# Kernel tuning notes

Hardware: AMD Instinct MI355X
Metric: run time of the kernel (lower is better)

## Reference

```python
import jax, jax.numpy as jnp
import numpy as np

N_HEAD = 16
N_EMBD = 1024
HEAD_DIM = N_EMBD // N_HEAD


def setup_inputs() -> dict:
    key = jax.random.key(0)
    k1, k2, k3 = jax.random.split(key, 3)
    B, T, C = 2, 2048, N_EMBD
    x = jax.random.normal(k1, (B, T, C), dtype=jnp.float32)
    # Linear weights stored as (in, out); torch nn.Linear weight is (out,in), y = x @ W.T.
    # We store the already-transposed form so reference does x @ w.
    w_attn = jax.random.normal(k2, (C, 3 * C), dtype=jnp.float32) * (1.0 / np.sqrt(C))
    w_proj = jax.random.normal(k3, (C, C), dtype=jnp.float32) * (1.0 / np.sqrt(C))
    return {"x": x, "w_attn": w_attn, "w_proj": w_proj}


def reference(x, w_attn, w_proj):
    B, T, C = x.shape
    qkv = x @ w_attn                          # [B,T,3C]
    q, k, v = jnp.split(qkv, 3, axis=2)
    # [B,T,C] -> [B,H,T,D]
    def heads(t):
        return t.reshape(B, T, N_HEAD, HEAD_DIM).transpose(0, 2, 1, 3)
    q, k, v = heads(q), heads(k), heads(v)
    scale = 1.0 / np.sqrt(HEAD_DIM)
    att = jnp.einsum('bhqd,bhkd->bhqk', q, k) * scale  # [B,H,T,T]
    causal = jnp.tril(jnp.ones((T, T), dtype=bool))
    att = jnp.where(causal, att, -jnp.inf)
    att = jax.nn.softmax(att, axis=-1)
    y = jnp.einsum('bhqk,bhkd->bhqd', att, v)          # [B,H,T,D]
    y = y.transpose(0, 2, 1, 3).reshape(B, T, C)
    return y @ w_proj
```

## Files before the change

### kernel.cpp

```cpp
#include <hip/hip_runtime.h>
#include <hip/hip_bf16.h>
#include <stdint.h>

typedef unsigned short u16;
typedef unsigned int u32;
typedef unsigned long long u64;
typedef float f32x4 __attribute__((ext_vector_type(4)));
typedef float f32x16 __attribute__((ext_vector_type(16)));
typedef short bf16x8 __attribute__((ext_vector_type(8)));
typedef u32 u32x4 __attribute__((ext_vector_type(4)));

#define MFMA(a, b, c) __builtin_amdgcn_mfma_f32_16x16x32_bf16((a), (b), (c), 0, 0, 0)
#define MFMA32(a, b, c) __builtin_amdgcn_mfma_f32_32x32x16_bf16((a), (b), (c), 0, 0, 0)

__device__ __forceinline__ void gll16(const void* g, void* lds) {
  __builtin_amdgcn_global_load_lds(
      (const __attribute__((address_space(1))) u32*)(uintptr_t)g,
      (__attribute__((address_space(3))) u32*)(uintptr_t)lds, 16, 0, 0);
}

__device__ __forceinline__ u16 f2b(float f) {
  union { __hip_bfloat16 h; u16 u; } cv;
  cv.h = __float2bfloat16(f);
  return cv.u;
}
__device__ __forceinline__ float b2f(u16 b) {
  union { u32 u; float f; } cv;
  cv.u = (u32)b << 16;
  return cv.f;
}
__device__ __forceinline__ u32 cvtpk(float lo, float hi) {
  u32 r;
  asm("v_cvt_pk_bf16_f32 %0, %1, %2" : "=v"(r) : "v"(lo), "v"(hi));
  return r;
}

__device__ __forceinline__ int sw(int r) { return ((r ^ (r >> 3)) & 7) << 4; }

__global__ __launch_bounds__(256) void k_cvt(const float* __restrict__ in,
                                             u16* __restrict__ out, int n4) {
  int i = blockIdx.x * 256 + threadIdx.x;
  if (i >= n4) return;
  const float4 v = reinterpret_cast<const float4*>(in)[i];
  u32 lo = (u32)f2b(v.x) | ((u32)f2b(v.y) << 16);
  u32 hi = (u32)f2b(v.z) | ((u32)f2b(v.w) << 16);
  reinterpret_cast<uint2*>(out)[i] = make_uint2(lo, hi);
}

__global__ __launch_bounds__(256) void k_trcvt(const float* __restrict__ in,
                                               u16* __restrict__ out, int R, int C) {
  __shared__ float tile[64][65];
  const int tid = threadIdx.x;
  const int r0 = blockIdx.y * 64, c0 = blockIdx.x * 64;
  const int tr = tid >> 4;
  const int tc4 = (tid & 15) * 4;
#pragma unroll
  for (int i = 0; i < 4; ++i) {
    const float4 v = *reinterpret_cast<const float4*>(
        &in[(size_t)(r0 + i * 16 + tr) * C + c0 + tc4]);
    tile[i * 16 + tr][tc4 + 0] = v.x;
    tile[i * 16 + tr][tc4 + 1] = v.y;
    tile[i * 16 + tr][tc4 + 2] = v.z;
    tile[i * 16 + tr][tc4 + 3] = v.w;
  }
  __syncthreads();
#pragma unroll
  for (int i = 0; i < 4; ++i) {
    const int c = i * 16 + tr;
    const int r4 = tc4;
    u32 lo = (u32)f2b(tile[r4 + 0][c]) | ((u32)f2b(tile[r4 + 1][c]) << 16);
    u32 hi = (u32)f2b(tile[r4 + 2][c]) | ((u32)f2b(tile[r4 + 3][c]) << 16);
    *reinterpret_cast<uint2*>(&out[(size_t)(c0 + c) * R + r0 + r4]) =
        make_uint2(lo, hi);
  }
}

template <int F32OUT>
__global__ __launch_bounds__(256) void k_gemm(const u16* __restrict__ A,
                                              const u16* __restrict__ Bt,
                                              void* __restrict__ Cout,
                                              int M, int N, int K) {
  __shared__ u16 As[128 * 32];
  __shared__ u16 Bs[128 * 32];
  const int tid = threadIdx.x;
  const int lane = tid & 63;
  const int w = tid >> 6;
  const int wm = w >> 1, wn = w & 1;
  const int l15 = lane & 15, lg = lane >> 4;
  const int brow = blockIdx.y * 128;
  const int bcol = blockIdx.x * 128;

  f32x4 acc[4][4] = {};

  const int r0 = tid >> 2;
  const int k8 = (tid & 3) * 8;
  const u16* Ag0 = A + (size_t)(brow + r0) * K + k8;
  const u16* Ag1 = A + (size_t)(brow + 64 + r0) * K + k8;
  const u16* Bg0 = Bt + (size_t)(bcol + r0) * K + k8;
  const u16* Bg1 = Bt + (size_t)(bcol + 64 + r0) * K + k8;
  u16* Asl0 = As + tid * 8;
  u16* Asl1 = As + 2048 + tid * 8;
  u16* Bsl0 = Bs + tid * 8;
  u16* Bsl1 = Bs + 2048 + tid * 8;

  for (int k0 = 0; k0 < K; k0 += 32) {
    gll16(Ag0 + k0, Asl0);
    gll16(Ag1 + k0, Asl1);
    gll16(Bg0 + k0, Bsl0);
    gll16(Bg1 + k0, Bsl1);
    __syncthreads();
    bf16x8 a[4], b[4];
#pragma unroll
    for (int m = 0; m < 4; ++m)
      a[m] = *(const bf16x8*)&As[(wm * 64 + m * 16 + l15) * 32 + lg * 8];
#pragma unroll
    for (int n = 0; n < 4; ++n)
      b[n] = *(const bf16x8*)&Bs[(wn * 64 + n * 16 + l15) * 32 + lg * 8];
#pragma unroll
    for (int m = 0; m < 4; ++m)
#pragma unroll
      for (int n = 0; n < 4; ++n)
        acc[m][n] = MFMA(a[m], b[n], acc[m][n]);
    __syncthreads();
  }

#pragma unroll
  for (int m = 0; m < 4; ++m) {
    const int row = brow + wm * 64 + m * 16 + lg * 4;
#pragma unroll
    for (int n = 0; n < 4; ++n) {
      const int col = bcol + wn * 64 + n * 16 + l15;
#pragma unroll
      for (int r = 0; r < 4; ++r) {
        const float v = acc[m][n][r];
        if (F32OUT)
          ((float*)Cout)[(size_t)(row + r) * N + col] = v;
        else
          ((u16*)Cout)[(size_t)(row + r) * N + col] = f2b(v);
      }
    }
  }
}

__global__ __launch_bounds__(512, 1) void k_attn(const u16* __restrict__ qkv,
                                                 u16* __restrict__ y) {
  __shared__ u16 Kl[3][64 * 64];
  __shared__ u16 Vt[2][64 * 64];
  __shared__ float Om[4][64][33];
  __shared__ float Lm[4][2][32];
  const int tid = threadIdx.x;
  const int lane = tid & 63;
  const int w = tid >> 6;
  const int qsub = w & 3, tsub = w >> 2;
  const int l31 = lane & 31, hi = lane >> 5;

  const int lin = blockIdx.x;
  const int xcd = lin & 7;
  const int idx = lin >> 3;
  const int bh = xcd * 4 + (idx >> 3);
  const int pidx = idx & 7;
  const int b = bh >> 4, h = bh & 15;

  const u16* Qg = qkv + (size_t)(b * 2048) * 3072 + h * 64;
  const u16* Kg = Qg + 1024;
  const u16* Vg = Qg + 2048;

  const int srow = tid >> 3;
  const int scol = (((tid & 7) * 16) ^ sw(srow)) >> 1;
  const bool vstage = (tid < 256);
  const int t2 = (tid & 255) >> 3;
  const int d8 = (tid & 7) * 8;

  bf16x8 vone;
#pragma unroll
  for (int j = 0; j < 8; ++j) vone[j] = (short)0x3F80;

  const int trow = tsub * 32 + l31;
  int koff[4];
#pragma unroll
  for (int ks = 0; ks < 4; ++ks)
    koff[ks] = trow * 128 + (((ks * 16 + hi * 8) * 2) ^ sw(trow));
  int voff[2][2];
#pragma unroll
  for (int db = 0; db < 2; ++db) {
    const int dl = db * 32 + l31;
#pragma unroll
    for (int ks = 0; ks < 2; ++ks)
      voff[db][ks] = dl * 128 + (((tsub * 32 + ks * 16 + hi * 8) * 2) ^ sw(dl));
  }

  for (int pass = 0; pass < 2; ++pass) {
    const int qi = pass ? (15 - pidx) : pidx;
    const int nt = 2 * (qi + 1);
    const int qb = qi * 128;
    const int qrow = qb + qsub * 32 + l31;

    bf16x8 aq[4];
#pragma unroll
    for (int ks = 0; ks < 4; ++ks) {
      bf16x8 v = *(const bf16x8*)&Qg[(size_t)qrow * 3072 + ks * 16 + hi * 8];
#pragma unroll
      for (int j = 0; j < 8; ++j)
        v[j] = (short)f2b(b2f((u16)v[j]) * 0.18033688011112042f);
      aq[ks] = v;
    }

    f32x16 acc0 = {}, acc1 = {}, accl = {};

    bf16x8 va0, va1;
    {
      bf16x8 v00, v01;
      if (vstage) {
        v00 = *(const bf16x8*)&Vg[(size_t)(2 * t2) * 3072 + d8];
        v01 = *(const bf16x8*)&Vg[(size_t)(2 * t2 + 1) * 3072 + d8];
        va0 = *(const bf16x8*)&Vg[(size_t)(64 + 2 * t2) * 3072 + d8];
        va1 = *(const bf16x8*)&Vg[(size_t)(64 + 2 * t2 + 1) * 3072 + d8];
      }
      gll16(Kg + (size_t)srow * 3072 + scol, (u16*)Kl[0] + tid * 8);
      gll16(Kg + (size_t)(64 + srow) * 3072 + scol, (u16*)Kl[1] + tid * 8);
      if (vstage) {
#pragma unroll
        for (int j = 0; j < 8; ++j) {
          const int d = d8 + j;
          const u32 val = (u32)(u16)v00[j] | ((u32)(u16)v01[j] << 16);
          *(u32*)((char*)Vt[0] + ((d * 128 + t2 * 4) ^ sw(d))) = val;
        }
      }
    }
    asm volatile("s_waitcnt vmcnt(1) lgkmcnt(0)" ::: "memory");
    __builtin_amdgcn_s_barrier();
    __builtin_amdgcn_sched_barrier(0);

    const char* kR = (const char*)Kl[0];
    const char* kN = (const char*)Kl[1];
    char* kN2 = (char*)Kl[2];
    const char* vR = (const char*)Vt[0];
    char* vW = (char*)Vt[1];

    for (int t = 0; t < nt; ++t) {
      const int tf = (t + 2 < 31 ? t + 2 : 31);
      bf16x8 vf0, vf1;
      if (vstage) {
        vf0 = *(const bf16x8*)&Vg[(size_t)(tf * 64 + 2 * t2) * 3072 + d8];
        vf1 = *(const bf16x8*)&Vg[(size_t)(tf * 64 + 2 * t2 + 1) * 3072 + d8];
      }
      gll16(Kg + (size_t)(tf * 64 + srow) * 3072 + scol, (u16*)kN2 + tid * 8);

      f32x16 s = {};
#pragma unroll
      for (int ks = 0; ks < 4; ++ks) {
        const bf16x8 kf = *(const bf16x8*)(kR + koff[ks]);
        s = MFMA32(kf, aq[ks], s);
      }

      float p[16];
      if (t >= nt - 2) {
#pragma unroll
        for (int r = 0; r < 16; ++r) {
          const int kkg = t * 64 + tsub * 32 + (r & 3) + 8 * (r >> 2) + 4 * hi;
          p[r] = exp2f(kkg > qrow ? -1e30f : s[r]);
        }
      } else {
#pragma unroll
        for (int r = 0; r < 16; ++r) p[r] = exp2f(s[r]);
      }

      const u32 X0 = cvtpk(p[0], p[1]),   X1 = cvtpk(p[2], p[3]);
      const u32 X2 = cvtpk(p[4], p[5]),   X3 = cvtpk(p[6], p[7]);
      const u32 X4 = cvtpk(p[8], p[9]),   X5 = cvtpk(p[10], p[11]);
      const u32 X6 = cvtpk(p[12], p[13]), X7 = cvtpk(p[14], p[15]);
      const u32 sx0 = (u32)__shfl_xor((int)X0, 32);
      const u32 sx1 = (u32)__shfl_xor((int)X1, 32);
      const u32 sx2 = (u32)__shfl_xor((int)X2, 32);
      const u32 sx3 = (u32)__shfl_xor((int)X3, 32);
      const u32 sx4 = (u32)__shfl_xor((int)X4, 32);
      const u32 sx5 = (u32)__shfl_xor((int)X5, 32);
      const u32 sx6 = (u32)__shfl_xor((int)X6, 32);
      const u32 sx7 = (u32)__shfl_xor((int)X7, 32);
      union { u32x4 u; bf16x8 h; } c0, c1;
      c0.u[0] = hi ? sx2 : X0;
      c0.u[1] = hi ? sx3 : X1;
      c0.u[2] = hi ? X2 : sx0;
      c0.u[3] = hi ? X3 : sx1;
      c1.u[0] = hi ? sx6 : X4;
      c1.u[1] = hi ? sx7 : X5;
      c1.u[2] = hi ? X6 : sx4;
      c1.u[3] = hi ? X7 : sx5;
      const bf16x8 pb0 = c0.h, pb1 = c1.h;

      accl = MFMA32(vone, pb0, accl);
      accl = MFMA32(vone, pb1, accl);
      const bf16x8 vb00 = *(const bf16x8*)(vR + voff[0][0]);
      const bf16x8 vb01 = *(const bf16x8*)(vR + voff[0][1]);
      const bf16x8 vb10 = *(const bf16x8*)(vR + voff[1][0]);
      const bf16x8 vb11 = *(const bf16x8*)(vR + voff[1][1]);
      acc0 = MFMA32(vb00, pb0, acc0);
      acc0 = MFMA32(vb01, pb1, acc0);
      acc1 = MFMA32(vb10, pb0, acc1);
      acc1 = MFMA32(vb11, pb1, acc1);

      if (vstage && t < nt - 1) {
#pragma unroll
        for (int j = 0; j < 8; ++j) {
          const int d = d8 + j;
          const u32 val = (u32)(u16)va0[j] | ((u32)(u16)va1[j] << 16);
          *(u32*)(vW + ((d * 128 + t2 * 4) ^ sw(d))) = val;
        }
      }
      va0 = vf0; va1 = vf1;
      const char* kt = kR; kR = kN; kN = kN2; kN2 = (char*)kt;
      char* vt_ = (char*)vR; vR = vW; vW = vt_;

      asm volatile("s_waitcnt vmcnt(1) lgkmcnt(0)" ::: "memory");
      __builtin_amdgcn_s_barrier();
      __builtin_amdgcn_sched_barrier(0);
    }

    asm volatile("s_waitcnt vmcnt(0) lgkmcnt(0)" ::: "memory");
    __builtin_amdgcn_s_barrier();
    __builtin_amdgcn_sched_barrier(0);

    if (tsub == 1) {
#pragma unroll
      for (int r = 0; r < 16; ++r) {
        const int d = (r & 3) + 8 * (r >> 2) + 4 * hi;
        Om[qsub][d][l31] = acc0[r];
        Om[qsub][32 + d][l31] = acc1[r];
      }
      Lm[qsub][1][l31] = accl[0];
    } else {
      Lm[qsub][0][l31] = accl[0];
    }
    __syncthreads();
    if (tsub == 0) {
      const float linv = 1.0f / (Lm[qsub][0][l31] + Lm[qsub][1][l31]);
#pragma unroll
      for (int r = 0; r < 16; ++r) {
        const int d = (r & 3) + 8 * (r >> 2) + 4 * hi;
        Om[qsub][d][l31] = (acc0[r] + Om[qsub][d][l31]) * linv;
        Om[qsub][32 + d][l31] = (acc1[r] + Om[qsub][32 + d][l31]) * linv;
      }
    }
    __syncthreads();
    {
      const int qloc = tid >> 2;
      const int dgr = (tid & 3) * 16;
      const size_t yo = (size_t)(b * 2048 + qb + qloc) * 1024 + h * 64 + dgr;
      u32 o[8];
#pragma unroll
      for (int jj = 0; jj < 8; ++jj)
        o[jj] = cvtpk(Om[qloc >> 5][dgr + 2 * jj][qloc & 31],
                      Om[qloc >> 5][dgr + 2 * jj + 1][qloc & 31]);
      u32x4 s0 = {o[0], o[1], o[2], o[3]};
      u32x4 s1 = {o[4], o[5], o[6], o[7]};
      *(u32x4*)&y[yo] = s0;
      *(u32x4*)&y[yo + 8] = s1;
    }
    __syncthreads();
  }
}

extern "C" void kernel_launch(void* const* d_in, const int* in_sizes, int n_in,
                              void* d_out, int out_size, void* d_ws, size_t ws_size,
                              hipStream_t stream) {
  const float* x  = (const float*)d_in[0];
  const float* wa = (const float*)d_in[1];
  const float* wp = (const float*)d_in[2];
  float* out = (float*)d_out;

  u16* xb  = (u16*)d_ws;
  u16* wat = xb + (size_t)4096 * 1024;
  u16* wpt = wat + (size_t)3072 * 1024;
  u16* qkv = wpt + (size_t)1024 * 1024;
  u16* yb  = qkv + (size_t)4096 * 3072;

  k_cvt<<<4096, 256, 0, stream>>>(x, xb, 4096 * 1024 / 4);
  k_trcvt<<<dim3(3072 / 64, 1024 / 64), 256, 0, stream>>>(wa, wat, 1024, 3072);
  k_trcvt<<<dim3(1024 / 64, 1024 / 64), 256, 0, stream>>>(wp, wpt, 1024, 1024);

  k_gemm<0><<<dim3(3072 / 128, 4096 / 128), 256, 0, stream>>>(xb, wat, qkv, 4096, 3072, 1024);

  k_attn<<<256, 512, 0, stream>>>(qkv, yb);

  k_gemm<1><<<dim3(1024 / 128, 4096 / 128), 256, 0, stream>>>(yb, wpt, out, 4096, 1024, 1024);
}
```

Measured before the change: 125.5 us.

## Add specialized 256x192 pipelined QKV GEMM kernel with one tile per CU

Replaces the generic 128x128 QKV projection GEMM (768 blocks of 256 threads) with a dedicated kernel that uses 256x192 tiles, 512 threads and 256 blocks, so each CU gets exactly one tile. It double-buffers LDS via async global-to-LDS loads spread across the MFMA phases, uses setprio around the MFMA bursts, and remaps block IDs per XCD. The aim is more data reuse per block, global loads that overlap compute, and no tail wave. In exchange it uses a large LDS footprint and more accumulator registers, and the kernel is hardcoded to these shapes.

```diff
diff --git a/kernel.cpp b/kernel.cpp
--- a/kernel.cpp
+++ b/kernel.cpp
@@ -138,6 +138,116 @@
         else
           ((u16*)Cout)[(size_t)(row + r) * N + col] = f2b(v);
       }
+    }
+  }
+}
+
+__global__ __launch_bounds__(512, 1) void k_gemm1(const u16* __restrict__ A,
+                                                  const u16* __restrict__ Bt,
+                                                  u16* __restrict__ C) {
+  __shared__ u16 As[2][256 * 64];
+  __shared__ u16 Bs[2][192 * 64];
+  const int tid = threadIdx.x;
+  const int lane = tid & 63;
+  const int w = tid >> 6;
+  const int wm = w >> 2, wn = w & 3;
+  const int l15 = lane & 15, lg = lane >> 4;
+
+  const int bid = blockIdx.x;
+  const int lin = (bid & 7) * 32 + (bid >> 3);
+  const int bm = lin >> 4, bn = lin & 15;
+  const size_t brow = (size_t)bm * 256, bcol = (size_t)bn * 192;
+
+  const int sr = tid >> 3;
+  const int scb = (tid & 7) * 16;
+  const int gcol = (scb ^ sw(sr)) >> 1;
+  const u16* Ag[4];
+#pragma unroll
+  for (int i = 0; i < 4; ++i) Ag[i] = A + (brow + i * 64 + sr) * 1024 + gcol;
+  const u16* Bg[3];
+#pragma unroll
+  for (int i = 0; i < 3; ++i) Bg[i] = Bt + (bcol + i * 64 + sr) * 1024 + gcol;
+
+  f32x4 acc[8][3] = {};
+
+#pragma unroll
+  for (int i = 0; i < 4; ++i) gll16(Ag[i], (char*)As[0] + i * 8192 + tid * 16);
+#pragma unroll
+  for (int i = 0; i < 3; ++i) gll16(Bg[i], (char*)Bs[0] + i * 8192 + tid * 16);
+  asm volatile("s_waitcnt vmcnt(0) lgkmcnt(0)" ::: "memory");
+  __builtin_amdgcn_s_barrier();
+  __builtin_amdgcn_sched_barrier(0);
+
+  for (int kt = 0; kt < 16; ++kt) {
+    const int cur = kt & 1;
+    const char* as = (const char*)As[cur];
+    const char* bs = (const char*)Bs[cur];
+    char* asn = (char*)As[cur ^ 1];
+    char* bsn = (char*)Bs[cur ^ 1];
+    const bool more = (kt + 1 < 16);
+    const int ko = (kt + 1) * 64;
+
+    bf16x8 bfr[3][2];
+#pragma unroll
+    for (int n = 0; n < 3; ++n) {
+      const int row = wn * 48 + n * 16 + l15;
+#pragma unroll
+      for (int kh = 0; kh < 2; ++kh)
+        bfr[n][kh] = *(const bf16x8*)(bs + row * 128 +
+                                      ((kh * 64 + lg * 16) ^ sw(row)));
+    }
+#define GPHASE(MB, STAGE_A, STAGE_B, LAST)                                    \
+    {                                                                         \
+      bf16x8 af[2][2];                                                        \
+      _Pragma("unroll")                                                       \
+      for (int mm = 0; mm < 2; ++mm) {                                        \
+        const int row = wm * 128 + (MB + mm) * 16 + l15;                      \
+        _Pragma("unroll")                                                     \
+        for (int kh = 0; kh < 2; ++kh)                                        \
+          af[mm][kh] = *(const bf16x8*)(as + row * 128 +                      \
+                                        ((kh * 64 + lg * 16) ^ sw(row)));     \
+      }                                                                       \
+      if (STAGE_A && more) {                                                  \
+        _Pragma("unroll")                                                     \
+        for (int i = 0; i < 4; ++i)                                           \
+          gll16(Ag[i] + ko, asn + i * 8192 + tid * 16);                       \
+      }                                                                       \
+      if (STAGE_B && more) {                                                  \
+        _Pragma("unroll")                                                     \
+        for (int i = 0; i < 3; ++i)                                           \
+          gll16(Bg[i] + ko, bsn + i * 8192 + tid * 16);                       \
+      }                                                                       \
+      __builtin_amdgcn_s_setprio(1);                                          \
+      _Pragma("unroll")                                                       \
+      for (int mm = 0; mm < 2; ++mm)                                          \
+        _Pragma("unroll")                                                     \
+        for (int n = 0; n < 3; ++n) {                                         \
+          acc[MB + mm][n] = MFMA(af[mm][0], bfr[n][0], acc[MB + mm][n]);      \
+          acc[MB + mm][n] = MFMA(af[mm][1], bfr[n][1], acc[MB + mm][n]);      \
+        }                                                                     \
+      __builtin_amdgcn_s_setprio(0);                                          \
+      if (LAST) {                                                             \
+        asm volatile("s_waitcnt vmcnt(0) lgkmcnt(0)" ::: "memory");           \
+      }                                                                       \
+      __builtin_amdgcn_s_barrier();                                           \
+    }
+    GPHASE(0, 1, 0, 0)
+    GPHASE(2, 0, 1, 0)
+    GPHASE(4, 0, 0, 0)
+    GPHASE(6, 0, 0, 1)
+#undef GPHASE
+    __builtin_amdgcn_sched_barrier(0);
+  }
+
+#pragma unroll
+  for (int m = 0; m < 8; ++m) {
+    const size_t row = brow + wm * 128 + m * 16 + lg * 4;
+#pragma unroll
+    for (int n = 0; n < 3; ++n) {
+      const size_t col = bcol + wn * 48 + n * 16 + l15;
+#pragma unroll
+      for (int r = 0; r < 4; ++r)
+        C[(row + r) * 3072 + col] = f2b(acc[m][n][r]);
     }
   }
 }
@@ -378,7 +488,7 @@
   k_trcvt<<<dim3(3072 / 64, 1024 / 64), 256, 0, stream>>>(wa, wat, 1024, 3072);
   k_trcvt<<<dim3(1024 / 64, 1024 / 64), 256, 0, stream>>>(wp, wpt, 1024, 1024);
 
-  k_gemm<0><<<dim3(3072 / 128, 4096 / 128), 256, 0, stream>>>(xb, wat, qkv, 4096, 3072, 1024);
+  k_gemm1<<<256, 512, 0, stream>>>(xb, wat, qkv);
 
   k_attn<<<256, 512, 0, stream>>>(qkv, yb);
 
```

Result: faster. 119.0 us (-5.1%).
